# Kernel optimization log

Hardware: AMD Instinct MI355X
Metric: run time of the kernel (lower is better)

## Reference

```python
import jax, jax.numpy as jnp
import numpy as np

H, CM, CS = 8, 8, 16  # num_heads, hidden mv channels, hidden scalar channels

# grade of each of the 16 basis blades of Cl(1,3): 1; e0..e3; e01..e23; e012..e123; e0123
GRADE = np.array([0, 1, 1, 1, 1, 2, 2, 2, 2, 2, 2, 3, 3, 3, 3, 4])
# blade metric signs (product of per-index metric diag(+,-,-,-)) used in the invariant inner product
ETA = np.array([1., 1., -1., -1., -1., -1., -1., -1., 1., 1., 1., 1., 1., 1., -1., -1.], dtype=np.float32)


def equi_linear(mv, s, w_mv, w_s2mv, w_mv2s, w_s):
    # w_mv: (5, out_mv, in_mv) grade-projection weights -> expand to per-component (16, out, in)
    wfull = w_mv[GRADE]
    mv_out = jnp.einsum('...ix,xoi->...ox', mv, wfull)
    mv_out = mv_out.at[..., 0].add(s @ w_s2mv.T)           # scalars feed grade-0 component
    s_out = s @ w_s.T + mv[..., 0] @ w_mv2s.T              # grade-0 component feeds scalars
    return mv_out, s_out


def split_heads_mv(x):  # (b, n, C*H, 16) -> (b, H, n, C, 16); channel idx = c*H + h
    b, n = x.shape[0], x.shape[1]
    return jnp.moveaxis(x.reshape(b, n, CM, H, 16), -2, -4)


def split_heads_s(x):  # (b, n, C*H) -> (b, H, n, C)
    b, n = x.shape[0], x.shape[1]
    return jnp.moveaxis(x.reshape(b, n, CS, H), -1, -3)


def reference(multivectors_kv, multivectors_q, scalars_kv, scalars_q,
              w_mv_q, w_s2mv_q, w_mv2s_q, w_s_q,
              w_mv_kv, w_s2mv_kv, w_mv2s_kv, w_s_kv,
              w_mv_o, w_s2mv_o, w_mv2s_o, w_s_o,
              head_scale):
    q_mv, q_s = equi_linear(multivectors_q, scalars_q, w_mv_q, w_s2mv_q, w_mv2s_q, w_s_q)
    kv_mv, kv_s = equi_linear(multivectors_kv, scalars_kv, w_mv_kv, w_s2mv_kv, w_mv2s_kv, w_s_kv)
    k_mv, v_mv = jnp.split(kv_mv, 2, axis=-2)
    k_s, v_s = jnp.split(kv_s, 2, axis=-1)
    q_mv, k_mv, v_mv = split_heads_mv(q_mv), split_heads_mv(k_mv), split_heads_mv(v_mv)
    q_s, k_s, v_s = split_heads_s(q_s), split_heads_s(k_s), split_heads_s(v_s)
    # geometric attention: Lorentz-invariant mv inner product + scalar dot product
    qf = (q_mv * ETA).reshape(*q_mv.shape[:-2], CM * 16)
    kf = k_mv.reshape(*k_mv.shape[:-2], CM * 16)
    vf = v_mv.reshape(*v_mv.shape[:-2], CM * 16)
    scale = 1.0 / float(np.sqrt(16 * CM + CS))
    scores = (jnp.einsum('bhqd,bhkd->bhqk', qf, kf)
              + jnp.einsum('bhqc,bhkc->bhqk', q_s, k_s)) * scale
    attn = jax.nn.softmax(scores, axis=-1)                 # (b, H, nq, nkv)
    h_mv = jnp.einsum('bhqk,bhkd->bhqd', attn, vf).reshape(*q_mv.shape[:-2], CM, 16)
    h_s = jnp.einsum('bhqk,bhkc->bhqc', attn, v_s)
    h_mv = h_mv * head_scale[:, None, None, None]
    h_s = h_s * head_scale[:, None, None]
    # merge heads: channel idx = h*CM + c
    h_mv = jnp.moveaxis(h_mv, -4, -3)
    h_mv = h_mv.reshape(*h_mv.shape[:-3], H * CM, 16)
    h_s = jnp.moveaxis(h_s, -3, -2)
    h_s = h_s.reshape(*h_s.shape[:-2], H * CS)
    return equi_linear(h_mv, h_s, w_mv_o, w_s2mv_o, w_mv2s_o, w_s_o)


def setup_inputs() -> dict:
    key = jax.random.key(0)
    ks = jax.random.split(key, 17)
    B, NQ, NKV = 4, 2048, 2048
    IN_MV, IN_S, OUT_MV, OUT_S = 16, 32, 16, 32

    def w(k, shape, fan_in):
        return jax.random.normal(k, shape, jnp.float32) / np.sqrt(fan_in).astype(np.float32)

    return {
        'multivectors_kv': jax.random.normal(ks[0], (B, NKV, IN_MV, 16), jnp.float32),
        'multivectors_q': jax.random.normal(ks[1], (B, NQ, IN_MV, 16), jnp.float32),
        'scalars_kv': jax.random.normal(ks[2], (B, NKV, IN_S), jnp.float32),
        'scalars_q': jax.random.normal(ks[3], (B, NQ, IN_S), jnp.float32),
        'w_mv_q': w(ks[4], (5, H * CM, IN_MV), IN_MV),
        'w_s2mv_q': w(ks[5], (H * CM, IN_S), IN_S),
        'w_mv2s_q': w(ks[6], (H * CS, IN_MV), IN_MV),
        'w_s_q': w(ks[7], (H * CS, IN_S), IN_S),
        'w_mv_kv': w(ks[8], (5, 2 * H * CM, IN_MV), IN_MV),
        'w_s2mv_kv': w(ks[9], (2 * H * CM, IN_S), IN_S),
        'w_mv2s_kv': w(ks[10], (2 * H * CS, IN_MV), IN_MV),
        'w_s_kv': w(ks[11], (2 * H * CS, IN_S), IN_S),
        'w_mv_o': w(ks[12], (5, OUT_MV, H * CM), H * CM),
        'w_s2mv_o': w(ks[13], (OUT_MV, H * CS), H * CS),
        'w_mv2s_o': w(ks[14], (OUT_S, H * CM), H * CM),
        'w_s_o': w(ks[15], (OUT_S, H * CS), H * CS),
        'head_scale': jnp.ones((H,), jnp.float32),
    }
```

## Files before the change

kernel.cpp:

```cpp
#include <hip/hip_runtime.h>
#include <math.h>


typedef float f32x4 __attribute__((ext_vector_type(4)));
typedef __bf16 bf16x8 __attribute__((ext_vector_type(8)));
typedef unsigned short u16;
typedef unsigned int u32;

#define QSCALE 0.120224586740747f
#define DEFER_THR 11.541560f

__device__ __forceinline__ u32 pack2(float a, float b) {
  u32 ua = __builtin_bit_cast(u32, a);
  u32 ub = __builtin_bit_cast(u32, b);
  ua = (ua + 0x7fffu + ((ua >> 16) & 1u)) >> 16;
  ub = (ub + 0x7fffu + ((ub >> 16) & 1u)) >> 16;
  return ua | (ub << 16);
}
__device__ __forceinline__ u16 bf16of(float a) { return (u16)(pack2(a, 0.f) & 0xffffu); }

__device__ __forceinline__ u32 cvtpk(float lo, float hi) {
  u32 r;
  asm("v_cvt_pk_bf16_f32 %0, %1, %2" : "=v"(r) : "v"(lo), "v"(hi));
  return r;
}
__device__ __forceinline__ float lo16f(u32 w) { return __builtin_bit_cast(float, w << 16); }
__device__ __forceinline__ float hi16f(u32 w) { return __builtin_bit_cast(float, w & 0xffff0000u); }

__device__ __forceinline__ f32x4 mfma_bf16(uint4 a, uint4 b, f32x4 c) {
  return __builtin_amdgcn_mfma_f32_16x16x32_bf16(
      __builtin_bit_cast(bf16x8, a), __builtin_bit_cast(bf16x8, b), c, 0, 0, 0);
}

__device__ __forceinline__ uint2 tr16(u32 addr) {
  uint2 r;
  asm volatile("ds_read_b64_tr_b16 %0, %1" : "=v"(r) : "v"(addr));
  return r;
}

__device__ __forceinline__ void glds16(const void* g, void* l) {
  __builtin_amdgcn_global_load_lds((const __attribute__((address_space(1))) void*)g,
                                   (__attribute__((address_space(3))) void*)l, 16, 0, 0);
}

__global__ __launch_bounds__(256) void k_proj_q(
    const float* __restrict__ mv, const float* __restrict__ sc,
    const float* __restrict__ w_mv, const float* __restrict__ w_s2mv,
    const float* __restrict__ w_mv2s, const float* __restrict__ w_s,
    u16* __restrict__ qf)
{
  __shared__ u16 qs[8*8*168];
  const int t = threadIdx.x;
  const int tok0 = blockIdx.x * 8;
  const int b0 = tok0 >> 11, n0 = tok0 & 2047;

  if (t < 128) {
    const int o = t & 63, h2 = t >> 6;
    float wreg[3][16];
    #pragma unroll
    for (int j = 0; j < 3; ++j)
      #pragma unroll
      for (int i = 0; i < 16; ++i)
        wreg[j][i] = w_mv[(((h2*2 + j)*64) + o)*16 + i];
    float ws2[32];
    if (h2 == 0)
      #pragma unroll
      for (int j = 0; j < 32; ++j) ws2[j] = w_s2mv[o*32 + j];
    const int c = o >> 3, hh = o & 7;
    for (int tk = 0; tk < 8; ++tk) {
      const float* L  = &mv[(size_t)(tok0+tk)*256];
      const float* Ls = &sc[(size_t)(tok0+tk)*32];
      float acc[8] = {0,0,0,0,0,0,0,0};
      if (h2 == 0) {
        #pragma unroll
        for (int i = 0; i < 16; ++i) {
          const float w0 = wreg[0][i], w1 = wreg[1][i], w2 = wreg[2][i];
          const float4 A = *(const float4*)&L[i*16];
          const float4 Bv = *(const float4*)&L[i*16 + 4];
          acc[0] += A.x*w0;  acc[1] += A.y*w1;  acc[2] += A.z*w1;  acc[3] += A.w*w1;
          acc[4] += Bv.x*w1; acc[5] += Bv.y*w2; acc[6] += Bv.z*w2; acc[7] += Bv.w*w2;
        }
        float a0 = 0.f;
        #pragma unroll
        for (int j4 = 0; j4 < 8; ++j4) {
          const float4 s4 = *(const float4*)&Ls[j4*4];
          a0 += s4.x*ws2[j4*4] + s4.y*ws2[j4*4+1] + s4.z*ws2[j4*4+2] + s4.w*ws2[j4*4+3];
        }
        acc[0] += a0;
        acc[0] *= QSCALE; acc[1] *= QSCALE;
        #pragma unroll
        for (int xx = 2; xx < 8; ++xx) acc[xx] *= -QSCALE;
      } else {
        #pragma unroll
        for (int i = 0; i < 16; ++i) {
          const float w0 = wreg[0][i], w1 = wreg[1][i], w2 = wreg[2][i];
          const float4 A = *(const float4*)&L[i*16 + 8];
          const float4 Bv = *(const float4*)&L[i*16 + 12];
          acc[0] += A.x*w0;  acc[1] += A.y*w0;  acc[2] += A.z*w0;  acc[3] += A.w*w1;
          acc[4] += Bv.x*w1; acc[5] += Bv.y*w1; acc[6] += Bv.z*w1; acc[7] += Bv.w*w2;
        }
        #pragma unroll
        for (int xx = 0; xx < 6; ++xx) acc[xx] *= QSCALE;
        acc[6] *= -QSCALE; acc[7] *= -QSCALE;
      }
      uint4 u; u.x = pack2(acc[0],acc[1]); u.y = pack2(acc[2],acc[3]);
      u.z = pack2(acc[4],acc[5]); u.w = pack2(acc[6],acc[7]);
      *(uint4*)&qs[(tk*8 + hh)*168 + c*16 + h2*8] = u;
    }
  } else {
    const int o2 = t - 128;
    float wsv[32], wm2[16];
    #pragma unroll
    for (int j = 0; j < 32; ++j) wsv[j] = w_s[o2*32 + j];
    #pragma unroll
    for (int i = 0; i < 16; ++i) wm2[i] = w_mv2s[o2*16 + i];
    const int cs = o2 >> 3, hh = o2 & 7;
    for (int tk = 0; tk < 8; ++tk) {
      const float* L  = &mv[(size_t)(tok0+tk)*256];
      const float* Ls = &sc[(size_t)(tok0+tk)*32];
      float a = 0.f;
      #pragma unroll
      for (int j4 = 0; j4 < 8; ++j4) {
        const float4 s4 = *(const float4*)&Ls[j4*4];
        a += s4.x*wsv[j4*4] + s4.y*wsv[j4*4+1] + s4.z*wsv[j4*4+2] + s4.w*wsv[j4*4+3];
      }
      #pragma unroll
      for (int i = 0; i < 16; ++i) a += L[i*16]*wm2[i];
      qs[(tk*8 + hh)*168 + 128 + cs] = bf16of(a * QSCALE);
    }
  }
  __syncthreads();
  for (int idx = t; idx < 8*8*20; idx += 256) {
    const int hh = idx / 160, rem = idx - hh*160;
    const int tk = rem / 20, u = rem - tk*20;
    uint4 v = (u < 18) ? *(const uint4*)&qs[(tk*8 + hh)*168 + u*8] : uint4{0,0,0,0};
    *(uint4*)(qf + ((size_t)(b0*8 + hh)*2048 + n0 + tk)*160 + u*8) = v;
  }
}

__global__ __launch_bounds__(512) void k_proj_kv(
    const float* __restrict__ mv, const float* __restrict__ sc,
    const float* __restrict__ w_mv, const float* __restrict__ w_s2mv,
    const float* __restrict__ w_mv2s, const float* __restrict__ w_s,
    u16* __restrict__ kf, u16* __restrict__ vf)
{
  __shared__ u16 kvs[2*8*8*168];
  const int t = threadIdx.x;
  const int tok0 = blockIdx.x * 8;
  const int b0 = tok0 >> 11, n0 = tok0 & 2047;

  if (t < 256) {
    const int o = t & 127, h2 = t >> 7;
    float wreg[3][16];
    #pragma unroll
    for (int j = 0; j < 3; ++j)
      #pragma unroll
      for (int i = 0; i < 16; ++i)
        wreg[j][i] = w_mv[(((h2*2 + j)*128) + o)*16 + i];
    float ws2[32];
    if (h2 == 0)
      #pragma unroll
      for (int j = 0; j < 32; ++j) ws2[j] = w_s2mv[o*32 + j];
    const int isv = o >> 6, oo = o & 63;
    const int c = oo >> 3, hh = oo & 7;
    u16* stg = &kvs[isv*8*8*168];
    for (int tk = 0; tk < 8; ++tk) {
      const float* L  = &mv[(size_t)(tok0+tk)*256];
      const float* Ls = &sc[(size_t)(tok0+tk)*32];
      float acc[8] = {0,0,0,0,0,0,0,0};
      if (h2 == 0) {
        #pragma unroll
        for (int i = 0; i < 16; ++i) {
          const float w0 = wreg[0][i], w1 = wreg[1][i], w2 = wreg[2][i];
          const float4 A = *(const float4*)&L[i*16];
          const float4 Bv = *(const float4*)&L[i*16 + 4];
          acc[0] += A.x*w0;  acc[1] += A.y*w1;  acc[2] += A.z*w1;  acc[3] += A.w*w1;
          acc[4] += Bv.x*w1; acc[5] += Bv.y*w2; acc[6] += Bv.z*w2; acc[7] += Bv.w*w2;
        }
        float a0 = 0.f;
        #pragma unroll
        for (int j4 = 0; j4 < 8; ++j4) {
          const float4 s4 = *(const float4*)&Ls[j4*4];
          a0 += s4.x*ws2[j4*4] + s4.y*ws2[j4*4+1] + s4.z*ws2[j4*4+2] + s4.w*ws2[j4*4+3];
        }
        acc[0] += a0;
      } else {
        #pragma unroll
        for (int i = 0; i < 16; ++i) {
          const float w0 = wreg[0][i], w1 = wreg[1][i], w2 = wreg[2][i];
          const float4 A = *(const float4*)&L[i*16 + 8];
          const float4 Bv = *(const float4*)&L[i*16 + 12];
          acc[0] += A.x*w0;  acc[1] += A.y*w0;  acc[2] += A.z*w0;  acc[3] += A.w*w1;
          acc[4] += Bv.x*w1; acc[5] += Bv.y*w1; acc[6] += Bv.z*w1; acc[7] += Bv.w*w2;
        }
      }
      uint4 u; u.x = pack2(acc[0],acc[1]); u.y = pack2(acc[2],acc[3]);
      u.z = pack2(acc[4],acc[5]); u.w = pack2(acc[6],acc[7]);
      *(uint4*)&stg[(tk*8 + hh)*168 + c*16 + h2*8] = u;
    }
  } else {
    const int o2 = t - 256;
    float wsv[32], wm2[16];
    #pragma unroll
    for (int j = 0; j < 32; ++j) wsv[j] = w_s[o2*32 + j];
    #pragma unroll
    for (int i = 0; i < 16; ++i) wm2[i] = w_mv2s[o2*16 + i];
    const int isv = o2 >> 7, oo2 = o2 & 127;
    const int cs = oo2 >> 3, hh = oo2 & 7;
    u16* stg = &kvs[isv*8*8*168];
    for (int tk = 0; tk < 8; ++tk) {
      const float* L  = &mv[(size_t)(tok0+tk)*256];
      const float* Ls = &sc[(size_t)(tok0+tk)*32];
      float a = 0.f;
      #pragma unroll
      for (int j4 = 0; j4 < 8; ++j4) {
        const float4 s4 = *(const float4*)&Ls[j4*4];
        a += s4.x*wsv[j4*4] + s4.y*wsv[j4*4+1] + s4.z*wsv[j4*4+2] + s4.w*wsv[j4*4+3];
      }
      #pragma unroll
      for (int i = 0; i < 16; ++i) a += L[i*16]*wm2[i];
      stg[(tk*8 + hh)*168 + 128 + cs] = bf16of(a);
    }
  }
  __syncthreads();
  for (int idx = t; idx < 2560; idx += 512) {
    const int isv = idx / 1280;
    const int r = idx - isv*1280;
    const int hh = r / 160, rem = r - hh*160;
    const int tk = rem / 20, u = rem - tk*20;
    uint4 v;
    if (u < 18)               v = *(const uint4*)&kvs[isv*8*8*168 + (tk*8 + hh)*168 + u*8];
    else if (u == 18 && isv)  v = uint4{0x3F80u, 0, 0, 0};
    else                      v = uint4{0, 0, 0, 0};
    u16* base = isv ? vf : kf;
    *(uint4*)(base + ((size_t)(b0*8 + hh)*2048 + n0 + tk)*160 + u*8) = v;
  }
}

__global__ __launch_bounds__(256, 2) void k_attn(
    const u16* __restrict__ qf, const u16* __restrict__ kf,
    const u16* __restrict__ vf, const float* __restrict__ hsc,
    u16* __restrict__ ho)
{
  __shared__ __align__(16) char smem[81920];

  const int orig = blockIdx.x;
  const int bid = (orig & 7) * 64 + (orig >> 3);
  const int qt = bid & 15;
  const int bh = bid >> 4;
  const int h  = bh & 7;
  const int t  = threadIdx.x;
  const int w  = t >> 6;
  const int lane = t & 63;
  const int qi = lane & 15;
  const int hi = lane >> 4;

  const char* kgB = (const char*)(kf + (size_t)bh * 2048 * 160);
  const char* vgB = (const char*)(vf + (size_t)bh * 2048 * 160);
  const u16* qg = qf + ((size_t)bh * 2048 + qt*128 + w*32) * 160;
  const float hsv = hsc[h];

  uint4 qfr0[5], qfr1[5];
  #pragma unroll
  for (int dc = 0; dc < 5; ++dc) {
    qfr0[dc] = *(const uint4*)(qg + (size_t)qi*160 + dc*32 + hi*8);
    qfr1[dc] = *(const uint4*)(qg + (size_t)(16 + qi)*160 + dc*32 + hi*8);
  }

  f32x4 o0[10], o1[10];
  #pragma unroll
  for (int d = 0; d < 10; ++d) { o0[d] = f32x4{0,0,0,0}; o1[d] = f32x4{0,0,0,0}; }
  float m0 = -INFINITY, m1 = -INFINITY;

  int soff[10];
  if (w < 2) {
    #pragma unroll
    for (int j = 0; j < 10; ++j) soff[j] = w*10240 + j*1024 + lane*16;
  } else {
    #pragma unroll
    for (int j = 0; j < 10; ++j) {
      const int p = (w-2)*10240 + j*1024 + lane*16;
      const int kblk = p / 5120, r1 = p - kblk*5120;
      const int dblk = r1 >> 9, r2 = r1 & 511;
      const int krow = r2 >> 5, dhalf = (r2 >> 4) & 1;
      soff[j] = (kblk*16 + krow)*320 + dblk*32 + dhalf*16;
    }
  }

  #define STAGE(KT, BUF) do {                                              \
    char* base_ = smem + (BUF)*40960;                                      \
    if (w < 2) {                                                           \
      const char* src_ = kgB + (size_t)(KT)*20480;                         \
      _Pragma("unroll")                                                    \
      for (int j = 0; j < 10; ++j)                                         \
        glds16(src_ + soff[j], base_ + w*10240 + j*1024);                  \
    } else {                                                               \
      const char* src_ = vgB + (size_t)(KT)*20480;                         \
      char* vb_ = base_ + 20480 + (w-2)*10240;                             \
      _Pragma("unroll")                                                    \
      for (int j = 0; j < 10; ++j)                                         \
        glds16(src_ + soff[j], vb_ + j*1024);                              \
    }                                                                      \
  } while (0)

  STAGE(0, 0);
  __syncthreads();

  for (int kt = 0; kt < 32; ++kt) {
    const int buf = kt & 1;
    if (kt < 31) STAGE(kt+1, buf^1);

    const char* KsB = smem + buf*40960;
    const u32 VoffB = (u32)(buf*40960 + 20480);

    f32x4 st0[4], st1[4];
    __builtin_amdgcn_s_setprio(1);
    #pragma unroll
    for (int ks = 0; ks < 4; ++ks) {
      st0[ks] = f32x4{0,0,0,0};
      st1[ks] = f32x4{0,0,0,0};
      #pragma unroll
      for (int dc = 0; dc < 5; ++dc) {
        const uint4 kf4 = *(const uint4*)(KsB + (ks*16 + qi)*320 + dc*64 + hi*16);
        st0[ks] = mfma_bf16(kf4, qfr0[dc], st0[ks]);
        st1[ks] = mfma_bf16(kf4, qfr1[dc], st1[ks]);
      }
    }
    __builtin_amdgcn_s_setprio(0);

    float pm0 = st0[0][0], pm1 = st1[0][0];
    #pragma unroll
    for (int ks = 0; ks < 4; ++ks)
      #pragma unroll
      for (int r = 0; r < 4; ++r) {
        pm0 = fmaxf(pm0, st0[ks][r]);
        pm1 = fmaxf(pm1, st1[ks][r]);
      }
    pm0 = fmaxf(pm0, __shfl_xor(pm0, 16)); pm0 = fmaxf(pm0, __shfl_xor(pm0, 32));
    pm1 = fmaxf(pm1, __shfl_xor(pm1, 16)); pm1 = fmaxf(pm1, __shfl_xor(pm1, 32));
    if (!__all(fmaxf(pm0 - m0, pm1 - m1) <= DEFER_THR)) {
      const float mn0 = fmaxf(m0, pm0), mn1 = fmaxf(m1, pm1);
      const float rs0 = exp2f(m0 - mn0), rs1 = exp2f(m1 - mn1);
      m0 = mn0; m1 = mn1;
      float rr0[4], rr1[4];
      #pragma unroll
      for (int r = 0; r < 4; ++r) {
        rr0[r] = __shfl(rs0, hi*4 + r);
        rr1[r] = __shfl(rs1, hi*4 + r);
      }
      #pragma unroll
      for (int d = 0; d < 10; ++d)
        #pragma unroll
        for (int r = 0; r < 4; ++r) { o0[d][r] *= rr0[r]; o1[d][r] *= rr1[r]; }
    }
    #pragma unroll
    for (int ks = 0; ks < 4; ++ks)
      #pragma unroll
      for (int r = 0; r < 4; ++r) {
        st0[ks][r] = exp2f(st0[ks][r] - m0);
        st1[ks][r] = exp2f(st1[ks][r] - m1);
      }

    uint4 pb0a, pb0b, pb1a, pb1b;
    pb0a.x = cvtpk(st0[0][0], st0[0][1]); pb0a.y = cvtpk(st0[0][2], st0[0][3]);
    pb0a.z = cvtpk(st0[1][0], st0[1][1]); pb0a.w = cvtpk(st0[1][2], st0[1][3]);
    pb0b.x = cvtpk(st0[2][0], st0[2][1]); pb0b.y = cvtpk(st0[2][2], st0[2][3]);
    pb0b.z = cvtpk(st0[3][0], st0[3][1]); pb0b.w = cvtpk(st0[3][2], st0[3][3]);
    pb1a.x = cvtpk(st1[0][0], st1[0][1]); pb1a.y = cvtpk(st1[0][2], st1[0][3]);
    pb1a.z = cvtpk(st1[1][0], st1[1][1]); pb1a.w = cvtpk(st1[1][2], st1[1][3]);
    pb1b.x = cvtpk(st1[2][0], st1[2][1]); pb1b.y = cvtpk(st1[2][2], st1[2][3]);
    pb1b.z = cvtpk(st1[3][0], st1[3][1]); pb1b.w = cvtpk(st1[3][2], st1[3][3]);

    const u32 vtb = VoffB + (u32)(hi*128 + (qi>>2)*32 + (qi&3)*8);
    __builtin_amdgcn_s_setprio(1);
    #pragma unroll
    for (int ds = 0; ds < 10; ++ds) {
      const u32 a0 = vtb + ds*512;
      uint2 t0 = tr16(a0);
      uint2 t1 = tr16(a0 + 5120);
      uint2 t2 = tr16(a0 + 10240);
      uint2 t3 = tr16(a0 + 15360);
      asm volatile("s_waitcnt lgkmcnt(0)" ::: "memory");
      __builtin_amdgcn_sched_barrier(0);
      const uint4 vb01{t0.x, t0.y, t1.x, t1.y};
      const uint4 vb23{t2.x, t2.y, t3.x, t3.y};
      o0[ds] = mfma_bf16(pb0a, vb01, o0[ds]);
      o0[ds] = mfma_bf16(pb0b, vb23, o0[ds]);
      o1[ds] = mfma_bf16(pb1a, vb01, o1[ds]);
      o1[ds] = mfma_bf16(pb1b, vb23, o1[ds]);
    }
    __builtin_amdgcn_s_setprio(0);

    __syncthreads();
  }

  float ir0[4], ir1[4];
  #pragma unroll
  for (int r = 0; r < 4; ++r) {
    ir0[r] = hsv / __shfl(o0[9][r], hi*16);
    ir1[r] = hsv / __shfl(o1[9][r], hi*16);
  }
  float (*Ol)[148] = reinterpret_cast<float(*)[148]>(smem);
  const size_t obase = ((size_t)bh*2048 + qt*128) * 144;
  #pragma unroll
  for (int f = 0; f < 2; ++f) {
    #pragma unroll
    for (int ds = 0; ds < 9; ++ds)
      #pragma unroll
      for (int r = 0; r < 4; ++r) {
        const int q = w*16 + hi*4 + r;
        const int loc = (ds < 8) ? (qi*8 + ds) : (128 + qi);
        Ol[q][loc] = (f ? o1[ds][r]*ir1[r] : o0[ds][r]*ir0[r]);
      }
    __syncthreads();
    for (int idx = t; idx < 64*18; idx += 256) {
      const int q = idx / 18, u = idx - q*18;
      const int grow = (q >> 4)*32 + f*16 + (q & 15);
      const float4 a = *(const float4*)&Ol[q][u*8];
      const float4 b = *(const float4*)&Ol[q][u*8 + 4];
      uint4 pk;
      pk.x = cvtpk(a.x, a.y); pk.y = cvtpk(a.z, a.w);
      pk.z = cvtpk(b.x, b.y); pk.w = cvtpk(b.z, b.w);
      *(uint4*)(ho + obase + (size_t)grow*144 + u*8) = pk;
    }
    __syncthreads();
  }
  #undef STAGE
}

__global__ __launch_bounds__(256) void k_out(
    const u16* __restrict__ ho,
    const float* __restrict__ w_mv, const float* __restrict__ w_s2mv,
    const float* __restrict__ w_mv2s, const float* __restrict__ w_s,
    float* __restrict__ out)
{
  constexpr int kGx[16] = {0,1,1,1,1,2,2,2,2,2,2,3,3,3,3,4};
  __shared__ float lh[8*1152];
  __shared__ float ob[256];
  __shared__ float csl[16];
  const int t = threadIdx.x;
  const int tok0 = blockIdx.x * 8;
  const int b0 = tok0 >> 11, n0 = tok0 & 2047;

  const int x = t >> 4, oB = t & 15;
  float4 wB[16];
  #pragma unroll
  for (int q = 0; q < 16; ++q)
    wB[q] = *(const float4*)&w_mv[(kGx[x]*16 + oB)*64 + q*4];

  float wC[16];
  float wD1[32], wD2[16];
  int oC = 0, pC = 0, oD = 0, pD = 0;
  if (t < 128) {
    oC = t >> 3; pC = t & 7;
    #pragma unroll
    for (int j = 0; j < 16; ++j) wC[j] = w_s2mv[oC*128 + pC*16 + j];
  } else {
    const int tt = t - 128;
    oD = tt >> 2; pD = tt & 3;
    #pragma unroll
    for (int j = 0; j < 32; ++j) wD1[j] = w_s[oD*128 + pD*32 + j];
    #pragma unroll
    for (int j = 0; j < 16; ++j) wD2[j] = w_mv2s[oD*64 + pD*16 + j];
  }

  for (int idx = t; idx < 1152; idx += 256) {
    const int tk = idx / 144, rem = idx - tk*144;
    const int hh = rem / 18, u8 = rem - hh*18;
    const uint4 v = *(const uint4*)&ho[(((size_t)(b0*8 + hh)*2048) + n0 + tk)*144 + u8*8];
    float* Lt = &lh[tk*1152];
    const int dst = (u8 < 16) ? (u8*64 + hh*8) : (1024 + hh*16 + (u8-16)*8);
    *(float4*)&Lt[dst]     = float4{lo16f(v.x), hi16f(v.x), lo16f(v.y), hi16f(v.y)};
    *(float4*)&Lt[dst + 4] = float4{lo16f(v.z), hi16f(v.z), lo16f(v.w), hi16f(v.w)};
  }
  __syncthreads();

  for (int tk = 0; tk < 8; ++tk) {
    const float* hp = &lh[tk*1152];
    float acc = 0.f;
    #pragma unroll
    for (int q = 0; q < 16; ++q) {
      const float4 hv = *(const float4*)&hp[x*64 + q*4];
      acc += hv.x*wB[q].x + hv.y*wB[q].y + hv.z*wB[q].z + hv.w*wB[q].w;
    }
    ob[t] = acc;
    if (t < 128) {
      float a = 0.f;
      #pragma unroll
      for (int j = 0; j < 16; ++j) a += hp[1024 + pC*16 + j]*wC[j];
      a += __shfl_xor(a, 1); a += __shfl_xor(a, 2); a += __shfl_xor(a, 4);
      if (pC == 0) csl[oC] = a;
    } else {
      float a = 0.f;
      #pragma unroll
      for (int j = 0; j < 32; ++j) a += hp[1024 + pD*32 + j]*wD1[j];
      #pragma unroll
      for (int j = 0; j < 16; ++j) a += hp[pD*16 + j]*wD2[j];
      a += __shfl_xor(a, 1); a += __shfl_xor(a, 2);
      if (pD == 0) out[2097152 + (size_t)(tok0 + tk)*32 + oD] = a;
    }
    __syncthreads();
    float v = ob[(t & 15)*16 + (t >> 4)];
    if ((t & 15) == 0) v += csl[t >> 4];
    out[(size_t)(tok0 + tk)*256 + t] = v;
    __syncthreads();
  }
}

extern "C" void kernel_launch(void* const* d_in, const int* in_sizes, int n_in,
                              void* d_out, int out_size, void* d_ws, size_t ws_size,
                              hipStream_t stream) {
  const float* mv_kv    = (const float*)d_in[0];
  const float* mv_q     = (const float*)d_in[1];
  const float* s_kv     = (const float*)d_in[2];
  const float* s_q      = (const float*)d_in[3];
  const float* w_mv_q   = (const float*)d_in[4];
  const float* w_s2mv_q = (const float*)d_in[5];
  const float* w_mv2s_q = (const float*)d_in[6];
  const float* w_s_q    = (const float*)d_in[7];
  const float* w_mv_kv   = (const float*)d_in[8];
  const float* w_s2mv_kv = (const float*)d_in[9];
  const float* w_mv2s_kv = (const float*)d_in[10];
  const float* w_s_kv    = (const float*)d_in[11];
  const float* w_mv_o   = (const float*)d_in[12];
  const float* w_s2mv_o = (const float*)d_in[13];
  const float* w_mv2s_o = (const float*)d_in[14];
  const float* w_s_o    = (const float*)d_in[15];
  const float* hscale   = (const float*)d_in[16];

  u16* qf = (u16*)d_ws;
  u16* kf = qf + 10485760;
  u16* vf = kf + 10485760;
  u16* ho = vf + 10485760;

  k_proj_q <<<1024, 256, 0, stream>>>(mv_q,  s_q,  w_mv_q,  w_s2mv_q,  w_mv2s_q,  w_s_q,  qf);
  k_proj_kv<<<1024, 512, 0, stream>>>(mv_kv, s_kv, w_mv_kv, w_s2mv_kv, w_mv2s_kv, w_s_kv, kf, vf);
  k_attn   <<< 512, 256, 0, stream>>>(qf, kf, vf, hscale, ho);
  k_out    <<<1024, 256, 0, stream>>>(ho, w_mv_o, w_s2mv_o, w_mv2s_o, w_s_o, (float*)d_out);
}
```

Before: 222.8 us.

## Read K directly from global memory and stage only V in LDS

Stops staging the K tile through shared memory. Each wave now loads its K fragments straight from global memory inside the QK^T MFMA loop, and only V is double-buffered in LDS, which halves the shared allocation. This removes LDS traffic and staging work for K and could allow more resident blocks. The cost is global or L2 latency sitting directly on the MFMA critical path, with no prefetch, and every wave re-reads the same K rows.

```diff
diff --git a/kernel.cpp b/kernel.cpp
--- a/kernel.cpp
+++ b/kernel.cpp
@@ -242,7 +242,7 @@
     const u16* __restrict__ vf, const float* __restrict__ hsc,
     u16* __restrict__ ho)
 {
-  __shared__ __align__(16) char smem[81920];
+  __shared__ __align__(16) char smem[40960];
 
   const int orig = blockIdx.x;
   const int bid = (orig & 7) * 64 + (orig >> 3);
@@ -255,7 +255,7 @@
   const int qi = lane & 15;
   const int hi = lane >> 4;
 
-  const char* kgB = (const char*)(kf + (size_t)bh * 2048 * 160);
+  const u16* kg  = kf + (size_t)bh * 2048 * 160;
   const char* vgB = (const char*)(vf + (size_t)bh * 2048 * 160);
   const u16* qg = qf + ((size_t)bh * 2048 + qt*128 + w*32) * 160;
   const float hsv = hsc[h];
@@ -272,35 +272,20 @@
   for (int d = 0; d < 10; ++d) { o0[d] = f32x4{0,0,0,0}; o1[d] = f32x4{0,0,0,0}; }
   float m0 = -INFINITY, m1 = -INFINITY;
 
-  int soff[10];
-  if (w < 2) {
-    #pragma unroll
-    for (int j = 0; j < 10; ++j) soff[j] = w*10240 + j*1024 + lane*16;
-  } else {
-    #pragma unroll
-    for (int j = 0; j < 10; ++j) {
-      const int p = (w-2)*10240 + j*1024 + lane*16;
-      const int kblk = p / 5120, r1 = p - kblk*5120;
-      const int dblk = r1 >> 9, r2 = r1 & 511;
-      const int krow = r2 >> 5, dhalf = (r2 >> 4) & 1;
-      soff[j] = (kblk*16 + krow)*320 + dblk*32 + dhalf*16;
-    }
+  int soff[5];
+  #pragma unroll
+  for (int j = 0; j < 5; ++j) {
+    const int r1 = j*1024 + lane*16;
+    const int dblk = r1 >> 9, krow = (r1 >> 5) & 15, dhalf = (r1 >> 4) & 1;
+    soff[j] = (w*16 + krow)*320 + dblk*32 + dhalf*16;
   }
 
   #define STAGE(KT, BUF) do {                                              \
-    char* base_ = smem + (BUF)*40960;                                      \
-    if (w < 2) {                                                           \
-      const char* src_ = kgB + (size_t)(KT)*20480;                         \
-      _Pragma("unroll")                                                    \
-      for (int j = 0; j < 10; ++j)                                         \
-        glds16(src_ + soff[j], base_ + w*10240 + j*1024);                  \
-    } else {                                                               \
-      const char* src_ = vgB + (size_t)(KT)*20480;                         \
-      char* vb_ = base_ + 20480 + (w-2)*10240;                             \
-      _Pragma("unroll")                                                    \
-      for (int j = 0; j < 10; ++j)                                         \
-        glds16(src_ + soff[j], vb_ + j*1024);                              \
-    }                                                                      \
+    char* vb_ = smem + (BUF)*20480 + w*5120;                               \
+    const char* src_ = vgB + (size_t)(KT)*20480;                           \
+    _Pragma("unroll")                                                      \
+    for (int j = 0; j < 5; ++j)                                            \
+      glds16(src_ + soff[j], vb_ + j*1024);                                \
   } while (0)
 
   STAGE(0, 0);
@@ -310,8 +295,7 @@
     const int buf = kt & 1;
     if (kt < 31) STAGE(kt+1, buf^1);
 
-    const char* KsB = smem + buf*40960;
-    const u32 VoffB = (u32)(buf*40960 + 20480);
+    const u32 VoffB = (u32)(buf*20480);
 
     f32x4 st0[4], st1[4];
     __builtin_amdgcn_s_setprio(1);
@@ -319,9 +303,10 @@
     for (int ks = 0; ks < 4; ++ks) {
       st0[ks] = f32x4{0,0,0,0};
       st1[ks] = f32x4{0,0,0,0};
+      const u16* krow = kg + (size_t)(kt*64 + ks*16 + qi)*160 + hi*8;
       #pragma unroll
       for (int dc = 0; dc < 5; ++dc) {
-        const uint4 kf4 = *(const uint4*)(KsB + (ks*16 + qi)*320 + dc*64 + hi*16);
+        const uint4 kf4 = *(const uint4*)(krow + dc*32);
         st0[ks] = mfma_bf16(kf4, qfr0[dc], st0[ks]);
         st1[ks] = mfma_bf16(kf4, qfr1[dc], st1[ks]);
       }
```

Result: slower. 272.6 us (+22.4%).
